# Performance work log

Hardware: AMD Instinct MI355X
Metric: run time of the kernel (lower is better)

The kernel has to match this reference:

```python
import jax, jax.numpy as jnp
import numpy as np

B, S, D, H, L, OUT = 64, 512, 256, 512, 2, 128


def setup_inputs() -> dict:
    key = jax.random.key(0)
    ks = jax.random.split(key, 11)
    s = 0.04  # ~1/sqrt(H) init scale, avoids gate saturation
    return {
        "x": jax.random.normal(ks[0], (B, S, D), jnp.float32),
        "W_ih0": jax.random.normal(ks[1], (4 * H, D), jnp.float32) * s,
        "W_hh0": jax.random.normal(ks[2], (4 * H, H), jnp.float32) * s,
        "b_ih0": jax.random.normal(ks[3], (4 * H,), jnp.float32) * s,
        "b_hh0": jax.random.normal(ks[4], (4 * H,), jnp.float32) * s,
        "W_ih1": jax.random.normal(ks[5], (4 * H, H), jnp.float32) * s,
        "W_hh1": jax.random.normal(ks[6], (4 * H, H), jnp.float32) * s,
        "b_ih1": jax.random.normal(ks[7], (4 * H,), jnp.float32) * s,
        "b_hh1": jax.random.normal(ks[8], (4 * H,), jnp.float32) * s,
        "fc_w": jax.random.normal(ks[9], (OUT, H), jnp.float32) * s,
        "fc_b": jax.random.normal(ks[10], (OUT,), jnp.float32) * s,
    }


def _lstm_layer(x_sbd, W_ih, W_hh, b_ih, b_hh):
    # x_sbd: [S, B, Din]. Precompute input contribution to all gates (one big GEMM).
    xg = jnp.einsum("sbd,gd->sbg", x_sbd, W_ih) + b_ih + b_hh  # [S, B, 4H]
    Hd = W_hh.shape[1]
    h0 = jnp.zeros((x_sbd.shape[1], Hd), x_sbd.dtype)
    c0 = jnp.zeros_like(h0)

    def step(carry, xg_t):
        h, c = carry
        gates = xg_t + h @ W_hh.T  # [B, 4H]
        i, f, g, o = jnp.split(gates, 4, axis=-1)  # PyTorch gate order i,f,g,o
        i, f, o = jax.nn.sigmoid(i), jax.nn.sigmoid(f), jax.nn.sigmoid(o)
        g = jnp.tanh(g)
        c = f * c + i * g
        h = o * jnp.tanh(c)
        return (h, c), h

    (_, _), hs = jax.lax.scan(step, (h0, c0), xg)
    return hs  # [S, B, H]


def reference(x, W_ih0, W_hh0, b_ih0, b_hh0, W_ih1, W_hh1, b_ih1, b_hh1, fc_w, fc_b):
    xs = jnp.transpose(x, (1, 0, 2))  # [S, B, D], time-major for scan
    h1 = _lstm_layer(xs, W_ih0, W_hh0, b_ih0, b_hh0)
    h2 = _lstm_layer(h1, W_ih1, W_hh1, b_ih1, b_hh1)
    last = h2[-1]  # [B, H] == out[:, -1, :]
    return last @ fc_w.T + fc_b  # [B, OUT]
```

## Files before the change

kernel.cpp:

```cpp
#include <hip/hip_runtime.h>

typedef unsigned long long u64;
typedef unsigned int u32;
typedef __attribute__((ext_vector_type(8))) short short8;
typedef __attribute__((ext_vector_type(4))) float floatx4;

#define Bc   64
#define Sc   512
#define Dc   256
#define Hc   512
#define OUTc 128

#define NWG  256
#define NTHR 512
#define NL0  128
#define JPW  16
#define NRW  64
#define KPB  1032

#define HQ   8192
#define WS_BYTES (4096 + 5 * HQ * 8)

__device__ __forceinline__ u64 cload8(const u64* p) {
    return __hip_atomic_load(p, __ATOMIC_RELAXED, __HIP_MEMORY_SCOPE_AGENT);
}
__device__ __forceinline__ void cstore4(u32* p, u32 v) {
    __hip_atomic_store(p, v, __ATOMIC_RELAXED, __HIP_MEMORY_SCOPE_AGENT);
}

__device__ __forceinline__ short bf16_rne(float f) {
    u32 u = __float_as_uint(f);
    u += 0x7fffu + ((u >> 16) & 1u);
    return (short)(u >> 16);
}
__device__ __forceinline__ float4 unpack4(u64 v) {
    u32 lo = (u32)v, hi = (u32)(v >> 32);
    float4 f;
    f.x = __uint_as_float(lo << 16);
    f.y = __uint_as_float(lo & 0xffff0000u);
    f.z = __uint_as_float(hi << 16);
    f.w = __uint_as_float(hi & 0xffff0000u);
    return f;
}
__device__ __forceinline__ u32 pack2_rne(float a, float b) {
    u32 ua = __float_as_uint(a), ub = __float_as_uint(b);
    ua += 0x7fffu + ((ua >> 16) & 1u);
    ub += 0x7fffu + ((ub >> 16) & 1u);
    return (ua >> 16) | (ub & 0xffff0000u);
}
__device__ __forceinline__ short8 frag2(u64 a, u64 b) {
    union { u64 u[2]; short8 s; } c; c.u[0] = a; c.u[1] = b; return c.s;
}

__device__ __forceinline__ void wait32(const u32* fbase, u32 target, int lane) {
    const u32* p = fbase + (lane & 31);
    for (;;) {
        u32 f = __hip_atomic_load(p, __ATOMIC_RELAXED, __HIP_MEMORY_SCOPE_AGENT);
        if (__all(f >= target)) return;
        __builtin_amdgcn_s_sleep(1);
    }
}
__device__ __forceinline__ void wait2(const u32* fa, u32 ta, const u32* fb, u32 tb, int lane) {
    const u32* pa = fa + (lane & 31);
    const u32* pb = fb + (lane & 31);
    for (;;) {
        u32 va = __hip_atomic_load(pa, __ATOMIC_RELAXED, __HIP_MEMORY_SCOPE_AGENT);
        u32 vb = __hip_atomic_load(pb, __ATOMIC_RELAXED, __HIP_MEMORY_SCOPE_AGENT);
        if (__all((va >= ta) && (vb >= tb))) return;
        __builtin_amdgcn_s_sleep(1);
    }
}
__device__ __forceinline__ void wait128(const u32* flags, u32 target, int lane) {
    const u32* p0 = flags + lane; const u32* p1 = flags + lane + 64;
    for (;;) {
        u32 f0 = __hip_atomic_load(p0, __ATOMIC_RELAXED, __HIP_MEMORY_SCOPE_AGENT);
        u32 f1 = __hip_atomic_load(p1, __ATOMIC_RELAXED, __HIP_MEMORY_SCOPE_AGENT);
        if (__all((f0 >= target) && (f1 >= target))) return;
        __builtin_amdgcn_s_sleep(1);
    }
}

__device__ __forceinline__ float sigmoidf_fast(float v) {
    return 1.0f / (1.0f + __expf(-v));
}
__device__ __forceinline__ float tanhf_fast(float v) {
    return 2.0f / (1.0f + __expf(-2.0f * v)) - 1.0f;
}

extern "C" __global__ void __launch_bounds__(NTHR)
lstm_persist(const float* __restrict__ x,
             const float* __restrict__ Wih0, const float* __restrict__ Whh0,
             const float* __restrict__ bih0, const float* __restrict__ bhh0,
             const float* __restrict__ Wih1, const float* __restrict__ Whh1,
             const float* __restrict__ bih1, const float* __restrict__ bhh1,
             const float* __restrict__ fcw, const float* __restrict__ fcb,
             float* __restrict__ out, float* __restrict__ wsf)
{
    __shared__ short Wl[NRW * KPB];
    __shared__ float red[2 * 4 * 16 * 20];

    u32* flags0 = (u32*)wsf;
    u32* flags1 = flags0 + 128;
    u64* h1b = (u64*)((char*)wsf + 4096);
    u64* h2b = h1b + 3 * HQ;

    const int wg  = blockIdx.x;
    const int tid = threadIdx.x;
    const bool isL1 = (wg >= NL0);
    const int wgl = isL1 ? wg - NL0 : wg;
    const int rg = wgl >> 2, bg = wgl & 3;
    const int j0 = rg * JPW;
    const int K  = isL1 ? 1024 : 768;
    const int KD = isL1 ? 512  : 256;

    {
        const float* Wi = isL1 ? Wih1 : Wih0;
        const float* Wh = isL1 ? Whh1 : Whh0;
        for (int r = 0; r < NRW; ++r) {
            const int row = (r >> 4) * Hc + j0 + (r & 15);
            for (int c = tid; c < K; c += NTHR) {
                float v = (c < KD) ? Wi[(size_t)row * KD + c] : Wh[(size_t)row * Hc + (c - KD)];
                Wl[r * KPB + c] = bf16_rne(v);
            }
        }
    }
    __syncthreads();

    const int w    = tid >> 6;
    const int lane = tid & 63;
    const int g    = w >> 1;
    const int half = w & 1;
    const int quad = lane >> 4;
    const int c16  = lane & 15;
    const int bglob = bg * 16 + c16;
    const int wrowb = (g * 16 + c16) * KPB;

    const int bl = tid & 15, jp = tid >> 4;
    float cst[2] = {0.0f, 0.0f};
    float bias2[2][4];
    {
        const float* bi = isL1 ? bih1 : bih0;
        const float* bh = isL1 ? bhh1 : bhh0;
#pragma unroll
        for (int jj2 = 0; jj2 < 2; ++jj2) {
            const int j = j0 + 2 * jp + jj2;
#pragma unroll
            for (int gg = 0; gg < 4; ++gg)
                bias2[jj2][gg] = bi[gg * Hc + j] + bh[gg * Hc + j];
        }
    }
    const int hsoff = ((j0 + 2 * jp) >> 2) * 128 + 2 * (bg * 16 + bl) + (jp & 1);

    u32* myflag = (isL1 ? flags1 : flags0) + bg * 32 + rg;
    const u32* f0b = flags0 + bg * 32;
    const u32* f1b = flags1 + bg * 32;

    for (int s = 0; s < Sc; ++s) {
        floatx4 acc = {0.0f, 0.0f, 0.0f, 0.0f};

        const int mW = s % 3;
        const int mR = (s + 2) % 3;

        if (!isL1) {
            {
                const float* xp = x + (size_t)bglob * Sc * Dc + (size_t)s * Dc
                                + half * 128 + quad * 8;
                float Xv[32];
#pragma unroll
                for (int i = 0; i < 8; ++i)
                    *(float4*)&Xv[4 * i] = *(const float4*)(xp + (i >> 1) * 32 + (i & 1) * 4);
#pragma unroll
                for (int i = 0; i < 4; ++i) {
                    short8 Bv;
#pragma unroll
                    for (int j = 0; j < 8; ++j) Bv[j] = bf16_rne(Xv[i * 8 + j]);
                    short8 A = *(const short8*)&Wl[wrowb + half * 128 + i * 32 + quad * 8];
                    acc = __builtin_amdgcn_mfma_f32_16x16x32_bf16(A, Bv, acc, 0, 0, 0);
                }
            }
            if (w == 0) wait2(f0b, (u32)s, f1b, (u32)(s >= 3 ? s - 2 : 0), lane);
            __syncthreads();
            {
                const u64* hb_ = h1b + (size_t)mR * HQ;
                u64 F[16];
#pragma unroll
                for (int i = 0; i < 8; ++i) {
                    const int q8 = (half * 64) + i * 8 + quad * 2;
                    F[2 * i]     = cload8(hb_ + (size_t)q8 * 64 + bglob);
                    F[2 * i + 1] = cload8(hb_ + (size_t)(q8 + 1) * 64 + bglob);
                }
#pragma unroll
                for (int i = 0; i < 8; ++i) {
                    short8 A = *(const short8*)&Wl[wrowb + 256 + half * 256 + i * 32 + quad * 8];
                    acc = __builtin_amdgcn_mfma_f32_16x16x32_bf16(A, frag2(F[2 * i], F[2 * i + 1]), acc, 0, 0, 0);
                }
            }
        } else {
            if (w == 0) wait2(f1b, (u32)s, f0b, (u32)(s + 1), lane);
            __syncthreads();
            {
                const u64* hb2 = h2b + (size_t)((s + 1) & 1) * HQ;
                const u64* hb1 = h1b + (size_t)mW * HQ;
                u64 F[32];
#pragma unroll
                for (int i = 0; i < 8; ++i) {
                    const int q8 = (half * 64) + i * 8 + quad * 2;
                    F[2 * i]     = cload8(hb2 + (size_t)q8 * 64 + bglob);
                    F[2 * i + 1] = cload8(hb2 + (size_t)(q8 + 1) * 64 + bglob);
                }
#pragma unroll
                for (int i = 0; i < 8; ++i) {
                    const int q8 = (half * 64) + i * 8 + quad * 2;
                    F[16 + 2 * i] = cload8(hb1 + (size_t)q8 * 64 + bglob);
                    F[17 + 2 * i] = cload8(hb1 + (size_t)(q8 + 1) * 64 + bglob);
                }
#pragma unroll
                for (int i = 0; i < 8; ++i) {
                    short8 A = *(const short8*)&Wl[wrowb + 512 + half * 256 + i * 32 + quad * 8];
                    acc = __builtin_amdgcn_mfma_f32_16x16x32_bf16(A, frag2(F[2 * i], F[2 * i + 1]), acc, 0, 0, 0);
                }
#pragma unroll
                for (int i = 0; i < 8; ++i) {
                    short8 A = *(const short8*)&Wl[wrowb + half * 256 + i * 32 + quad * 8];
                    acc = __builtin_amdgcn_mfma_f32_16x16x32_bf16(A, frag2(F[16 + 2 * i], F[17 + 2 * i]), acc, 0, 0, 0);
                }
            }
        }

        *(float4*)&red[((half * 4 + g) * 16 + c16) * 20 + quad * 4] =
            make_float4(acc[0], acc[1], acc[2], acc[3]);
        __syncthreads();

        if (tid < 128) {
            float hv[2];
#pragma unroll
            for (int jj2 = 0; jj2 < 2; ++jj2) {
                const int jl = 2 * jp + jj2;
                float gv[4];
#pragma unroll
                for (int gg = 0; gg < 4; ++gg)
                    gv[gg] = red[((0 + gg) * 16 + bl) * 20 + jl]
                           + red[((4 + gg) * 16 + bl) * 20 + jl] + bias2[jj2][gg];
                const float ig = sigmoidf_fast(gv[0]);
                const float fg = sigmoidf_fast(gv[1]);
                const float gt = tanhf_fast(gv[2]);
                const float og = sigmoidf_fast(gv[3]);
                cst[jj2] = fg * cst[jj2] + ig * gt;
                hv[jj2] = og * tanhf_fast(cst[jj2]);
            }
            u64* hb = isL1 ? (h2b + (size_t)(s & 1) * HQ)
                           : (h1b + (size_t)mW * HQ);
            cstore4((u32*)hb + hsoff, pack2_rne(hv[0], hv[1]));
        }
        __syncthreads();
        if (tid == 0)
            __hip_atomic_store(myflag, (u32)(s + 1), __ATOMIC_RELAXED, __HIP_MEMORY_SCOPE_AGENT);
    }

    if (wg < Bc) {
        if (w == 0) wait128(flags1, (u32)Sc, lane);
        __syncthreads();
        const int b = wg;
        const u64* h2 = h2b + (size_t)((Sc - 1) & 1) * HQ;
        const int o = tid & 127, q = tid >> 7;
        const float* wrow = fcw + (size_t)o * Hc;
        float a = 0.0f;
        for (int k4 = q * 32; k4 < q * 32 + 32; ++k4) {
            const float4 f = unpack4(cload8(h2 + (size_t)k4 * 64 + b));
            const float* wr = wrow + 4 * k4;
            a += f.x * wr[0] + f.y * wr[1] + f.z * wr[2] + f.w * wr[3];
        }
        __syncthreads();
        red[q * 128 + o] = a;
        __syncthreads();
        if (tid < OUTc)
            out[b * OUTc + tid] = red[tid] + red[128 + tid] + red[256 + tid] + red[384 + tid] + fcb[tid];
    }
}

extern "C" void kernel_launch(void* const* d_in, const int* in_sizes, int n_in,
                              void* d_out, int out_size, void* d_ws, size_t ws_size,
                              hipStream_t stream) {
    const float* x    = (const float*)d_in[0];
    const float* Wih0 = (const float*)d_in[1];
    const float* Whh0 = (const float*)d_in[2];
    const float* bih0 = (const float*)d_in[3];
    const float* bhh0 = (const float*)d_in[4];
    const float* Wih1 = (const float*)d_in[5];
    const float* Whh1 = (const float*)d_in[6];
    const float* bih1 = (const float*)d_in[7];
    const float* bhh1 = (const float*)d_in[8];
    const float* fcw  = (const float*)d_in[9];
    const float* fcb  = (const float*)d_in[10];
    float* out = (float*)d_out;
    float* wsf = (float*)d_ws;

    hipMemsetAsync(d_ws, 0, WS_BYTES, stream);

    lstm_persist<<<dim3(NWG), dim3(NTHR), 0, stream>>>(
        x, Wih0, Whh0, bih0, bhh0, Wih1, Whh1, bih1, bhh1, fcw, fcb, out, wsf);
}
```

Baseline: 2.047 ms.

## Replace flag-based step sync with tagged h-values and LDS-shared hidden state

Drops the per-workgroup flag arrays. Each stored bf16 hidden value now carries a 16-bit step tag in its low half, so consumers spin directly on the data until every tag matches, instead of polling flags and then loading the data. One wave group loads the hidden state once per step and stages it in LDS for all waves. Layer 1 prefetches its own recurrent state early to overlap the two loads. The h buffers go from triple to double buffering, backed by a separate layer-1-to-layer-0 progress counter. The cost is twice the bytes per hidden value, raw s_barrier use, and bounded spin loops that could read stale data on timeout.

New measurement: 2.573 ms. 25.7% more time.

```diff
diff --git a/kernel.cpp b/kernel.cpp
--- a/kernel.cpp
+++ b/kernel.cpp
@@ -13,79 +13,45 @@
 
 #define NWG  256
 #define NTHR 512
-#define NL0  128
 #define JPW  16
 #define NRW  64
 #define KPB  1032
-
-#define HQ   8192
-#define WS_BYTES (4096 + 5 * HQ * 8)
-
-__device__ __forceinline__ u64 cload8(const u64* p) {
-    return __hip_atomic_load(p, __ATOMIC_RELAXED, __HIP_MEMORY_SCOPE_AGENT);
-}
-__device__ __forceinline__ void cstore4(u32* p, u32 v) {
-    __hip_atomic_store(p, v, __ATOMIC_RELAXED, __HIP_MEMORY_SCOPE_AGENT);
-}
+#define SPIN  (1 << 13)
+#define SPINF (1 << 16)
+
+#define WAR_OFF  0
+#define H1T_OFF  1024
+#define H2T_OFF  (1024 + 262144)
+#define WS_BYTES (1024 + 2 * 262144)
 
 __device__ __forceinline__ short bf16_rne(float f) {
     u32 u = __float_as_uint(f);
     u += 0x7fffu + ((u >> 16) & 1u);
     return (short)(u >> 16);
 }
-__device__ __forceinline__ float4 unpack4(u64 v) {
-    u32 lo = (u32)v, hi = (u32)(v >> 32);
-    float4 f;
-    f.x = __uint_as_float(lo << 16);
-    f.y = __uint_as_float(lo & 0xffff0000u);
-    f.z = __uint_as_float(hi << 16);
-    f.w = __uint_as_float(hi & 0xffff0000u);
-    return f;
-}
-__device__ __forceinline__ u32 pack2_rne(float a, float b) {
-    u32 ua = __float_as_uint(a), ub = __float_as_uint(b);
-    ua += 0x7fffu + ((ua >> 16) & 1u);
-    ub += 0x7fffu + ((ub >> 16) & 1u);
-    return (ua >> 16) | (ub & 0xffff0000u);
-}
 __device__ __forceinline__ short8 frag2(u64 a, u64 b) {
     union { u64 u[2]; short8 s; } c; c.u[0] = a; c.u[1] = b; return c.s;
 }
-
-__device__ __forceinline__ void wait32(const u32* fbase, u32 target, int lane) {
-    const u32* p = fbase + (lane & 31);
-    for (;;) {
-        u32 f = __hip_atomic_load(p, __ATOMIC_RELAXED, __HIP_MEMORY_SCOPE_AGENT);
-        if (__all(f >= target)) return;
-        __builtin_amdgcn_s_sleep(1);
-    }
-}
-__device__ __forceinline__ void wait2(const u32* fa, u32 ta, const u32* fb, u32 tb, int lane) {
-    const u32* pa = fa + (lane & 31);
-    const u32* pb = fb + (lane & 31);
-    for (;;) {
-        u32 va = __hip_atomic_load(pa, __ATOMIC_RELAXED, __HIP_MEMORY_SCOPE_AGENT);
-        u32 vb = __hip_atomic_load(pb, __ATOMIC_RELAXED, __HIP_MEMORY_SCOPE_AGENT);
-        if (__all((va >= ta) && (vb >= tb))) return;
-        __builtin_amdgcn_s_sleep(1);
-    }
-}
-__device__ __forceinline__ void wait128(const u32* flags, u32 target, int lane) {
-    const u32* p0 = flags + lane; const u32* p1 = flags + lane + 64;
-    for (;;) {
-        u32 f0 = __hip_atomic_load(p0, __ATOMIC_RELAXED, __HIP_MEMORY_SCOPE_AGENT);
-        u32 f1 = __hip_atomic_load(p1, __ATOMIC_RELAXED, __HIP_MEMORY_SCOPE_AGENT);
-        if (__all((f0 >= target) && (f1 >= target))) return;
-        __builtin_amdgcn_s_sleep(1);
-    }
-}
-
 __device__ __forceinline__ float sigmoidf_fast(float v) {
     return 1.0f / (1.0f + __expf(-v));
 }
 __device__ __forceinline__ float tanhf_fast(float v) {
     return 2.0f / (1.0f + __expf(-2.0f * v)) - 1.0f;
 }
+__device__ __forceinline__ u64 al64(const u64* p) {
+    return __hip_atomic_load(p, __ATOMIC_RELAXED, __HIP_MEMORY_SCOPE_AGENT);
+}
+__device__ __forceinline__ u32 al32(const u32* p) {
+    return __hip_atomic_load(p, __ATOMIC_RELAXED, __HIP_MEMORY_SCOPE_AGENT);
+}
+__device__ __forceinline__ void as32(u32* p, u32 v) {
+    __hip_atomic_store(p, v, __ATOMIC_RELAXED, __HIP_MEMORY_SCOPE_AGENT);
+}
+#define LGKM0 do { asm volatile("s_waitcnt lgkmcnt(0)" ::: "memory"); } while (0)
+__device__ __forceinline__ void bar() {
+    asm volatile("s_barrier" ::: "memory");
+}
+#define MFMA16(A, B, C) __builtin_amdgcn_mfma_f32_16x16x32_bf16((A), (B), (C), 0, 0, 0)
 
 extern "C" __global__ void __launch_bounds__(NTHR)
 lstm_persist(const float* __restrict__ x,
@@ -97,17 +63,18 @@
              float* __restrict__ out, float* __restrict__ wsf)
 {
     __shared__ short Wl[NRW * KPB];
-    __shared__ float red[2 * 4 * 16 * 20];
-
-    u32* flags0 = (u32*)wsf;
-    u32* flags1 = flags0 + 128;
-    u64* h1b = (u64*)((char*)wsf + 4096);
-    u64* h2b = h1b + 3 * HQ;
+    __shared__ float red[8 * 16 * 20];
+    __shared__ u64 hshare[128 * 17];
+
+    char* wsb = (char*)wsf;
+    u32* war = (u32*)(wsb + WAR_OFF);
+    u64* h1t = (u64*)(wsb + H1T_OFF);
+    u64* h2t = (u64*)(wsb + H2T_OFF);
 
     const int wg  = blockIdx.x;
     const int tid = threadIdx.x;
-    const bool isL1 = (wg >= NL0);
-    const int wgl = isL1 ? wg - NL0 : wg;
+    const bool isL1 = wg >= 128;
+    const int wgl = isL1 ? wg - 128 : wg;
     const int rg = wgl >> 2, bg = wgl & 3;
     const int j0 = rg * JPW;
     const int K  = isL1 ? 1024 : 768;
@@ -126,14 +93,12 @@
     }
     __syncthreads();
 
-    const int w    = tid >> 6;
-    const int lane = tid & 63;
-    const int g    = w >> 1;
-    const int half = w & 1;
-    const int quad = lane >> 4;
-    const int c16  = lane & 15;
+    const int w = tid >> 6, lane = tid & 63;
+    const int g = w >> 1, half = w & 1;
+    const int quad = lane >> 4, c16 = lane & 15;
     const int bglob = bg * 16 + c16;
     const int wrowb = (g * 16 + c16) * KPB;
+    const size_t lofs = ((size_t)(half * 64 + quad * 16) * 64 + bglob) * 2;
 
     const int bl = tid & 15, jp = tid >> 4;
     float cst[2] = {0.0f, 0.0f};
@@ -149,17 +114,13 @@
                 bias2[jj2][gg] = bi[gg * Hc + j] + bh[gg * Hc + j];
         }
     }
-    const int hsoff = ((j0 + 2 * jp) >> 2) * 128 + 2 * (bg * 16 + bl) + (jp & 1);
-
-    u32* myflag = (isL1 ? flags1 : flags0) + bg * 32 + rg;
-    const u32* f0b = flags0 + bg * 32;
-    const u32* f1b = flags1 + bg * 32;
+    const size_t gofs = ((size_t)(rg * 4 + (jp >> 1)) * 64 + bg * 16 + bl) * 2 + (jp & 1);
+
+    u32 warv = 0;
 
     for (int s = 0; s < Sc; ++s) {
         floatx4 acc = {0.0f, 0.0f, 0.0f, 0.0f};
-
-        const int mW = s % 3;
-        const int mR = (s + 2) % 3;
+        u64 T2[32];
 
         if (!isL1) {
             {
@@ -173,63 +134,136 @@
                 for (int i = 0; i < 4; ++i) {
                     short8 Bv;
 #pragma unroll
-                    for (int j = 0; j < 8; ++j) Bv[j] = bf16_rne(Xv[i * 8 + j]);
-                    short8 A = *(const short8*)&Wl[wrowb + half * 128 + i * 32 + quad * 8];
-                    acc = __builtin_amdgcn_mfma_f32_16x16x32_bf16(A, Bv, acc, 0, 0, 0);
-                }
-            }
-            if (w == 0) wait2(f0b, (u32)s, f1b, (u32)(s >= 3 ? s - 2 : 0), lane);
-            __syncthreads();
-            {
-                const u64* hb_ = h1b + (size_t)mR * HQ;
-                u64 F[16];
+                    for (int jj = 0; jj < 8; ++jj) Bv[jj] = bf16_rne(Xv[i * 8 + jj]);
+                    acc = MFMA16(*(const short8*)&Wl[wrowb + half * 128 + i * 32 + quad * 8], Bv, acc);
+                }
+            }
+            if (g == 0 && s > 0) {
+                const u64* src = h1t + (size_t)((s + 1) & 1) * 16384 + lofs;
+                const u32 want = (u32)s & 0xffffu;
+                for (int it = 0;; ++it) {
+#pragma unroll
+                    for (int r = 0; r < 16; ++r) {
+                        T2[2 * r]     = al64(src + (size_t)r * 128);
+                        T2[2 * r + 1] = al64(src + (size_t)r * 128 + 1);
+                    }
+                    u32 bad = 0;
+#pragma unroll
+                    for (int r = 0; r < 32; ++r)
+                        bad |= ((u32)T2[r] ^ want) | ((u32)(T2[r] >> 32) ^ want);
+                    if (__all((bad & 0xffffu) == 0) || it > SPIN) break;
+                }
+#pragma unroll
+                for (int r = 0; r < 16; ++r) {
+                    u32 p0 = ((u32)T2[2 * r] >> 16)     | ((u32)(T2[2 * r] >> 32) & 0xffff0000u);
+                    u32 p1 = ((u32)T2[2 * r + 1] >> 16) | ((u32)(T2[2 * r + 1] >> 32) & 0xffff0000u);
+                    hshare[(half * 64 + quad * 16 + r) * 17 + c16] = ((u64)p1 << 32) | p0;
+                }
+                LGKM0;
+            }
+            if (w == 0 && s >= 2) {
+                const u32 need = (u32)(s - 1);
+                if (!__all(warv >= need)) {
+                    int it = 0;
+                    do { warv = al32(war + bg * 32 + (lane & 31)); }
+                    while (!__all(warv >= need) && ++it < SPIN);
+                }
+            }
+            bar();
+            if (s > 0) {
 #pragma unroll
                 for (int i = 0; i < 8; ++i) {
-                    const int q8 = (half * 64) + i * 8 + quad * 2;
-                    F[2 * i]     = cload8(hb_ + (size_t)q8 * 64 + bglob);
-                    F[2 * i + 1] = cload8(hb_ + (size_t)(q8 + 1) * 64 + bglob);
-                }
+                    const int q8 = half * 64 + i * 8 + quad * 2;
+                    u64 d0 = hshare[q8 * 17 + c16];
+                    u64 d1 = hshare[(q8 + 1) * 17 + c16];
+                    acc = MFMA16(*(const short8*)&Wl[wrowb + 256 + half * 256 + i * 32 + quad * 8],
+                                 frag2(d0, d1), acc);
+                }
+            }
+        } else {
+            if (g == 1 && s > 0) {
+                const u64* src = h2t + (size_t)((s + 1) & 1) * 16384 + lofs;
+#pragma unroll
+                for (int r = 0; r < 16; ++r) {
+                    T2[2 * r]     = al64(src + (size_t)r * 128);
+                    T2[2 * r + 1] = al64(src + (size_t)r * 128 + 1);
+                }
+            }
+            if (g == 0) {
+                const u64* src = h1t + (size_t)(s & 1) * 16384 + lofs;
+                const u32 want = (u32)(s + 1) & 0xffffu;
+                u64 T[32];
+                for (int it = 0;; ++it) {
+#pragma unroll
+                    for (int r = 0; r < 16; ++r) {
+                        T[2 * r]     = al64(src + (size_t)r * 128);
+                        T[2 * r + 1] = al64(src + (size_t)r * 128 + 1);
+                    }
+                    u32 bad = 0;
+#pragma unroll
+                    for (int r = 0; r < 32; ++r)
+                        bad |= ((u32)T[r] ^ want) | ((u32)(T[r] >> 32) ^ want);
+                    if (__all((bad & 0xffffu) == 0) || it > SPIN) break;
+                }
+#pragma unroll
+                for (int r = 0; r < 16; ++r) {
+                    u32 p0 = ((u32)T[2 * r] >> 16)     | ((u32)(T[2 * r] >> 32) & 0xffff0000u);
+                    u32 p1 = ((u32)T[2 * r + 1] >> 16) | ((u32)(T[2 * r + 1] >> 32) & 0xffff0000u);
+                    hshare[(half * 64 + quad * 16 + r) * 17 + c16] = ((u64)p1 << 32) | p0;
+                }
+                LGKM0;
+            }
+            bar();
+            if (tid == 256) as32(war + bg * 32 + rg, (u32)(s + 1));
+#pragma unroll
+            for (int i = 0; i < 8; ++i) {
+                const int q8 = half * 64 + i * 8 + quad * 2;
+                u64 d0 = hshare[q8 * 17 + c16];
+                u64 d1 = hshare[(q8 + 1) * 17 + c16];
+                acc = MFMA16(*(const short8*)&Wl[wrowb + half * 256 + i * 32 + quad * 8],
+                             frag2(d0, d1), acc);
+            }
+            LGKM0;
+            bar();
+            if (g == 1 && s > 0) {
+                const u64* src = h2t + (size_t)((s + 1) & 1) * 16384 + lofs;
+                const u32 want = (u32)s & 0xffffu;
+                for (int it = 0;; ++it) {
+                    u32 bad = 0;
+#pragma unroll
+                    for (int r = 0; r < 32; ++r)
+                        bad |= ((u32)T2[r] ^ want) | ((u32)(T2[r] >> 32) ^ want);
+                    if (__all((bad & 0xffffu) == 0) || it > SPIN) break;
+#pragma unroll
+                    for (int r = 0; r < 16; ++r) {
+                        T2[2 * r]     = al64(src + (size_t)r * 128);
+                        T2[2 * r + 1] = al64(src + (size_t)r * 128 + 1);
+                    }
+                }
+#pragma unroll
+                for (int r = 0; r < 16; ++r) {
+                    u32 p0 = ((u32)T2[2 * r] >> 16)     | ((u32)(T2[2 * r] >> 32) & 0xffff0000u);
+                    u32 p1 = ((u32)T2[2 * r + 1] >> 16) | ((u32)(T2[2 * r + 1] >> 32) & 0xffff0000u);
+                    hshare[(half * 64 + quad * 16 + r) * 17 + c16] = ((u64)p1 << 32) | p0;
+                }
+                LGKM0;
+            }
+            bar();
+            if (s > 0) {
 #pragma unroll
                 for (int i = 0; i < 8; ++i) {
-                    short8 A = *(const short8*)&Wl[wrowb + 256 + half * 256 + i * 32 + quad * 8];
-                    acc = __builtin_amdgcn_mfma_f32_16x16x32_bf16(A, frag2(F[2 * i], F[2 * i + 1]), acc, 0, 0, 0);
-                }
-            }
-        } else {
-            if (w == 0) wait2(f1b, (u32)s, f0b, (u32)(s + 1), lane);
-            __syncthreads();
-            {
-                const u64* hb2 = h2b + (size_t)((s + 1) & 1) * HQ;
-                const u64* hb1 = h1b + (size_t)mW * HQ;
-                u64 F[32];
-#pragma unroll
-                for (int i = 0; i < 8; ++i) {
-                    const int q8 = (half * 64) + i * 8 + quad * 2;
-                    F[2 * i]     = cload8(hb2 + (size_t)q8 * 64 + bglob);
-                    F[2 * i + 1] = cload8(hb2 + (size_t)(q8 + 1) * 64 + bglob);
-                }
-#pragma unroll
-                for (int i = 0; i < 8; ++i) {
-                    const int q8 = (half * 64) + i * 8 + quad * 2;
-                    F[16 + 2 * i] = cload8(hb1 + (size_t)q8 * 64 + bglob);
-                    F[17 + 2 * i] = cload8(hb1 + (size_t)(q8 + 1) * 64 + bglob);
-                }
-#pragma unroll
-                for (int i = 0; i < 8; ++i) {
-                    short8 A = *(const short8*)&Wl[wrowb + 512 + half * 256 + i * 32 + quad * 8];
-                    acc = __builtin_amdgcn_mfma_f32_16x16x32_bf16(A, frag2(F[2 * i], F[2 * i + 1]), acc, 0, 0, 0);
-                }
-#pragma unroll
-                for (int i = 0; i < 8; ++i) {
-                    short8 A = *(const short8*)&Wl[wrowb + half * 256 + i * 32 + quad * 8];
-                    acc = __builtin_amdgcn_mfma_f32_16x16x32_bf16(A, frag2(F[16 + 2 * i], F[17 + 2 * i]), acc, 0, 0, 0);
-                }
-            }
-        }
-
-        *(float4*)&red[((half * 4 + g) * 16 + c16) * 20 + quad * 4] =
-            make_float4(acc[0], acc[1], acc[2], acc[3]);
-        __syncthreads();
+                    const int q8 = half * 64 + i * 8 + quad * 2;
+                    u64 d0 = hshare[q8 * 17 + c16];
+                    u64 d1 = hshare[(q8 + 1) * 17 + c16];
+                    acc = MFMA16(*(const short8*)&Wl[wrowb + 512 + half * 256 + i * 32 + quad * 8],
+                                 frag2(d0, d1), acc);
+                }
+            }
+        }
+
+        *(floatx4*)&red[((half * 4 + g) * 16 + c16) * 20 + quad * 4] = acc;
+        LGKM0;
+        bar();
 
         if (tid < 128) {
             float hv[2];
@@ -239,7 +273,7 @@
                 float gv[4];
 #pragma unroll
                 for (int gg = 0; gg < 4; ++gg)
-                    gv[gg] = red[((0 + gg) * 16 + bl) * 20 + jl]
+                    gv[gg] = red[(gg * 16 + bl) * 20 + jl]
                            + red[((4 + gg) * 16 + bl) * 20 + jl] + bias2[jj2][gg];
                 const float ig = sigmoidf_fast(gv[0]);
                 const float fg = sigmoidf_fast(gv[1]);
@@ -248,33 +282,45 @@
                 cst[jj2] = fg * cst[jj2] + ig * gt;
                 hv[jj2] = og * tanhf_fast(cst[jj2]);
             }
-            u64* hb = isL1 ? (h2b + (size_t)(s & 1) * HQ)
-                           : (h1b + (size_t)mW * HQ);
-            cstore4((u32*)hb + hsoff, pack2_rne(hv[0], hv[1]));
-        }
-        __syncthreads();
-        if (tid == 0)
-            __hip_atomic_store(myflag, (u32)(s + 1), __ATOMIC_RELAXED, __HIP_MEMORY_SCOPE_AGENT);
+            const u32 tg = (u32)(s + 1) & 0xffffu;
+            const u32 lo = tg | ((u32)(unsigned short)bf16_rne(hv[0]) << 16);
+            const u32 hi = tg | ((u32)(unsigned short)bf16_rne(hv[1]) << 16);
+            u32* dst = (u32*)((isL1 ? h2t : h1t) + (size_t)(s & 1) * 16384 + gofs);
+            as32(dst, lo);
+            as32(dst + 1, hi);
+        }
+        bar();
     }
 
     if (wg < Bc) {
-        if (w == 0) wait128(flags1, (u32)Sc, lane);
         __syncthreads();
         const int b = wg;
-        const u64* h2 = h2b + (size_t)((Sc - 1) & 1) * HQ;
+        const u64* h2f = h2t + (size_t)((Sc - 1) & 1) * 16384;
+        const u32 want = (u32)Sc & 0xffffu;
         const int o = tid & 127, q = tid >> 7;
         const float* wrow = fcw + (size_t)o * Hc;
         float a = 0.0f;
         for (int k4 = q * 32; k4 < q * 32 + 32; ++k4) {
-            const float4 f = unpack4(cload8(h2 + (size_t)k4 * 64 + b));
+            const u64* p = h2f + ((size_t)k4 * 64 + b) * 2;
+            u64 t0, t1; int it = 0;
+            for (;;) {
+                t0 = al64(p); t1 = al64(p + 1);
+                u32 bad = (((u32)t0 ^ want) | ((u32)(t0 >> 32) ^ want)
+                         | ((u32)t1 ^ want) | ((u32)(t1 >> 32) ^ want)) & 0xffffu;
+                if (bad == 0 || ++it > SPINF) break;
+            }
             const float* wr = wrow + 4 * k4;
-            a += f.x * wr[0] + f.y * wr[1] + f.z * wr[2] + f.w * wr[3];
+            a += __uint_as_float((u32)t0 & 0xffff0000u)         * wr[0]
+               + __uint_as_float((u32)(t0 >> 32) & 0xffff0000u) * wr[1]
+               + __uint_as_float((u32)t1 & 0xffff0000u)         * wr[2]
+               + __uint_as_float((u32)(t1 >> 32) & 0xffff0000u) * wr[3];
         }
         __syncthreads();
         red[q * 128 + o] = a;
         __syncthreads();
         if (tid < OUTc)
-            out[b * OUTc + tid] = red[tid] + red[128 + tid] + red[256 + tid] + red[384 + tid] + fcb[tid];
+            out[b * OUTc + tid] = red[tid] + red[128 + tid] + red[256 + tid]
+                                + red[384 + tid] + fcb[tid];
     }
 }
 
```
